# Kernel optimization log

Measured on AMD Instinct MI355X. Metric: run time of the kernel, lower is better.

## Reference

```python
import jax, jax.numpy as jnp
import numpy as np

VOCAB, EMBED, HIDDEN = 50257, 256, 512
BATCH, SEQ = 4, 2048


def posneg(x):
    # max(0,x) - |min(0,x)|  (mathematically the identity, computed as written)
    return jnp.maximum(jnp.zeros_like(x), x) - jnp.abs(jnp.minimum(jnp.zeros_like(x), x))


def setup_inputs() -> dict:
    key = jax.random.key(0)
    ks = jax.random.split(key, 10)
    s = 0.02
    return {
        "token_ids": jax.random.randint(ks[0], (BATCH, SEQ), 0, VOCAB),
        "emb_table": jax.random.normal(ks[1], (VOCAB, EMBED), jnp.float32) * s,
        "W1": jax.random.normal(ks[2], (EMBED, HIDDEN), jnp.float32) * s,
        "b1": jax.random.normal(ks[3], (HIDDEN,), jnp.float32) * s,
        "Wq": jax.random.normal(ks[4], (HIDDEN, HIDDEN), jnp.float32) * s,
        "bq": jax.random.normal(ks[5], (HIDDEN,), jnp.float32) * s,
        "Wk": jax.random.normal(ks[6], (HIDDEN, HIDDEN), jnp.float32) * s,
        "bk": jax.random.normal(ks[7], (HIDDEN,), jnp.float32) * s,
        "Wv": jax.random.normal(ks[8], (HIDDEN, HIDDEN), jnp.float32) * s,
        "bv": jax.random.normal(ks[9], (HIDDEN,), jnp.float32) * s,
    }


def reference(token_ids, emb_table, W1, b1, Wq, bq, Wk, bk, Wv, bv):
    emb = emb_table[token_ids]                      # [B,S,E]
    emb = posneg(emb)
    hidden = posneg(emb) @ W1 + b1                  # [B,S,H]
    hidden = posneg(hidden)
    act = jax.nn.gelu(hidden, approximate=False)
    act = posneg(act)
    q = posneg(act) @ Wq + bq
    k = posneg(act) @ Wk + bk
    v = posneg(act) @ Wv + bv
    q, k, v = posneg(q), posneg(k), posneg(v)
    # scaled_dot_product_attention (single head, hand-rolled)
    q, k = posneg(q), posneg(k)
    scores = jnp.einsum("bsh,bth->bst", q, k)       # [B,S,S]
    scores = posneg(scores) / jnp.sqrt(jnp.float32(q.shape[-1]))
    attn = jax.nn.softmax(scores, axis=-1)
    attn = posneg(attn)
    v = posneg(v)
    out = jnp.einsum("bst,bth->bsh", attn, v)       # [B,S,H]
    return posneg(out)
```

## Files before the change

kernel.cpp:

```cpp
#include <hip/hip_runtime.h>
#include <math.h>


typedef unsigned short u16;
typedef u16   u16x8 __attribute__((ext_vector_type(8)));
typedef short s16x8 __attribute__((ext_vector_type(8)));
typedef float f32x4 __attribute__((ext_vector_type(4)));
typedef float f32x8 __attribute__((ext_vector_type(8)));

static __device__ __forceinline__ u16 f2bf(float f) {
    unsigned u = __builtin_bit_cast(unsigned, f);
    u = (u + 0x7fffu + ((u >> 16) & 1u)) >> 16;
    return (u16)u;
}
static __device__ __forceinline__ float bf2f(u16 h) {
    unsigned u = ((unsigned)h) << 16;
    return __builtin_bit_cast(float, u);
}

static __device__ __forceinline__ void gload_lds16(const u16* g, u16* l) {
    __builtin_amdgcn_global_load_lds(
        (const __attribute__((address_space(1))) void*)g,
        (__attribute__((address_space(3))) void*)l, 16, 0, 0);
}

__launch_bounds__(256)
__global__ void cvt_gather_k(const float* __restrict__ emb, const int* __restrict__ tok,
                             u16* __restrict__ dst)
{
    const int b = blockIdx.x;
    const int g = (b & 7) * 128 + (b >> 3);
    const int t = g * 2048 + threadIdx.x * 8;
    const int row = t >> 8;
    const int c8  = t & 255;
    f32x8 v = *(const f32x8*)(emb + (long)tok[row] * 256 + c8);
    u16x8 o;
#pragma unroll
    for (int j = 0; j < 8; ++j) o[j] = f2bf(v[j]);
    *(u16x8*)(dst + (long)row * 256 + c8) = o;
}

struct WArgs {
    const float* src[4];
    u16*         dst[4];
    int          K[4];
};

__launch_bounds__(256)
__global__ void transpose_w_k(WArgs wa)
{
    const int w = blockIdx.z;
    const float* W = wa.src[w];
    u16* WT = wa.dst[w];
    const int K = wa.K[w];
    const int c0 = blockIdx.x * 64;
    const int r0 = blockIdx.y * 64;
    if (r0 >= K) return;

    __shared__ float T[64][65];
    const int t = threadIdx.x;
    const int col = t & 63;
    const int rb  = t >> 6;

#pragma unroll
    for (int i = 0; i < 16; ++i)
        T[i * 4 + rb][col] = W[(long)(r0 + i * 4 + rb) * 512 + c0 + col];
    __syncthreads();
#pragma unroll
    for (int i = 0; i < 16; ++i) {
        const int orow = i * 4 + rb;
        WT[(long)(c0 + orow) * K + r0 + col] = f2bf(T[col][orow]);
    }
}

__launch_bounds__(256)
__global__ void transpose_v_k(const u16* __restrict__ v, u16* __restrict__ vT)
{
    const int b  = blockIdx.z;
    const int h0 = blockIdx.x * 64;
    const int t0 = blockIdx.y * 64;

    __shared__ u16 T[64][65];
    const int t = threadIdx.x;
    const int col = t & 63;
    const int rb  = t >> 6;

#pragma unroll
    for (int i = 0; i < 16; ++i) {
        const int row = i * 4 + rb;
        T[row][col] = v[(long)(b * 2048 + t0 + row) * 512 + h0 + col];
    }
    __syncthreads();
#pragma unroll
    for (int i = 0; i < 16; ++i) {
        const int orow = i * 4 + rb;
        vT[(long)b * (512 * 2048) + (long)(h0 + orow) * 2048 + t0 + col] = T[col][orow];
    }
}

struct GArgs {
    const u16* A; const u16* B; const float* bias; void* C;
    float* Cpart;
    u16 *qd, *kd, *vd;
    const float *bq, *bk, *bv;
    int K, lda, ldb, ldc;
    long strA, strB, strC;
    float scale;
};

template <int TM, int EPI, int CMODE, bool MX, bool SPLITK, bool XSW>
__launch_bounds__(256)
__global__ void gemm128(GArgs g)
{
    constexpr int BM  = TM * 32;
    constexpr int ASZ = BM * 32;
    constexpr int BSZ = 128 * 32;
    __shared__ u16 As[2 * ASZ];
    __shared__ u16 Bs[2 * BSZ];

    const int bz    = blockIdx.z;
    const int batch = SPLITK ? (bz >> 1) : bz;
    const int kh    = SPLITK ? (bz & 1) : 0;
    const u16* A = g.A + g.strA * batch + (SPLITK ? kh * 1024 : 0);
    const u16* B = g.B + g.strB * batch + (SPLITK ? kh * 1024 : 0);

    int m0, n0;
    if (XSW) {
        const int lid = blockIdx.y * gridDim.x + blockIdx.x;
        const int xcd = lid & 7;
        const int j   = lid >> 3;
        const int mper = gridDim.y >> 3;
        m0 = (xcd * mper + (j % mper)) * BM;
        n0 = (j / mper) * 128;
    } else {
        m0 = (MX ? blockIdx.x : blockIdx.y) * BM;
        n0 = (MX ? blockIdx.y : blockIdx.x) * 128;
    }

    const int t = threadIdx.x;
    const int w = t >> 6;
    const int lane = t & 63;
    const int quad = lane >> 4;
    const int l16  = lane & 15;
    const int wm = w >> 1, wn = w & 1;

    const int srow = w * 16 + (lane >> 2);
    const int skc  = (lane & 3) * 8;
    const u16* ga = A + (long)(m0 + srow) * g.lda + skc;
    const u16* gb = B + (long)(n0 + srow) * g.ldb + skc;
    const long a64 = (long)64 * g.lda;
    const long b64 = (long)64 * g.ldb;
    u16* lA = As + w * 512;
    u16* lB = Bs + w * 512;

    auto stage = [&](int buf, int k0) {
        u16* la = lA + buf * ASZ;
        u16* lb = lB + buf * BSZ;
        gload_lds16(ga + k0, la);
        if (TM == 4) gload_lds16(ga + a64 + k0, la + 2048);
        gload_lds16(gb + k0, lb);
        gload_lds16(gb + b64 + k0, lb + 2048);
    };

    f32x4 acc[TM][4] = {};
    const int K = SPLITK ? 1024 : g.K;

    stage(0, 0);
    int cur = 0;
    for (int k0 = 0; k0 < K; k0 += 32) {
        __syncthreads();
        if (k0 + 32 < K) stage(cur ^ 1, k0 + 32);

        const u16* as = As + cur * ASZ;
        const u16* bs = Bs + cur * BSZ;
        s16x8 af[TM], bf[4];
#pragma unroll
        for (int x = 0; x < TM; ++x)
            af[x] = *(const s16x8*)&as[(wm * (TM * 16) + x * 16 + l16) * 32 + quad * 8];
#pragma unroll
        for (int y = 0; y < 4; ++y)
            bf[y] = *(const s16x8*)&bs[(wn * 64 + y * 16 + l16) * 32 + quad * 8];
#pragma unroll
        for (int x = 0; x < TM; ++x)
#pragma unroll
            for (int y = 0; y < 4; ++y)
                acc[x][y] = __builtin_amdgcn_mfma_f32_16x16x32_bf16(af[x], bf[y], acc[x][y], 0, 0, 0);
        cur ^= 1;
    }

#pragma unroll
    for (int y = 0; y < 4; ++y) {
        const int col = n0 + wn * 64 + y * 16 + l16;
        float bval = 0.0f;
        if (CMODE == 2)
            bval = col < 512 ? g.bq[col] : (col < 1024 ? g.bk[col - 512] : g.bv[col - 1024]);
        else if (EPI >= 1)
            bval = g.bias[col];
#pragma unroll
        for (int x = 0; x < TM; ++x) {
#pragma unroll
            for (int r = 0; r < 4; ++r) {
                const int row = m0 + wm * (TM * 16) + x * 16 + quad * 4 + r;
                float v = acc[x][y][r] * g.scale + bval;
                if (EPI == 2) v = 0.5f * v * (1.0f + erff(v * 0.70710678118654752f));
                if (CMODE == 2) {
                    u16* dst = col < 512 ? g.qd : (col < 1024 ? g.kd : g.vd);
                    const int c = col & 511;
                    dst[(long)row * 512 + c] = f2bf(v);
                } else if (SPLITK) {
                    float* dst = kh ? g.Cpart : (float*)g.C;
                    dst[g.strC * batch + (long)row * g.ldc + col] = v;
                } else if (CMODE == 1) {
                    ((float*)g.C + g.strC * batch)[(long)row * g.ldc + col] = v;
                } else {
                    ((u16*)g.C + g.strC * batch)[(long)row * g.ldc + col] = f2bf(v);
                }
            }
        }
    }
}

__launch_bounds__(256)
__global__ void softmax_k(u16* __restrict__ sc)
{
    const long base = (long)blockIdx.x * 2048;
    const int t = threadIdx.x;
    const int wid = t >> 6, lane = t & 63;
    __shared__ float redm[4];
    __shared__ float reds[4];

    float v[8];
    float mx = -1e30f;
#pragma unroll
    for (int i = 0; i < 8; ++i) {
        v[i] = bf2f(sc[base + i * 256 + t]);
        mx = fmaxf(mx, v[i]);
    }
#pragma unroll
    for (int off = 32; off; off >>= 1) mx = fmaxf(mx, __shfl_xor(mx, off, 64));
    if (lane == 0) redm[wid] = mx;
    __syncthreads();
    const float bm = fmaxf(fmaxf(redm[0], redm[1]), fmaxf(redm[2], redm[3]));

    float s = 0.0f;
#pragma unroll
    for (int i = 0; i < 8; ++i) { v[i] = expf(v[i] - bm); s += v[i]; }
#pragma unroll
    for (int off = 32; off; off >>= 1) s += __shfl_xor(s, off, 64);
    if (lane == 0) reds[wid] = s;
    __syncthreads();
    const float inv = 1.0f / (reds[0] + reds[1] + reds[2] + reds[3]);

#pragma unroll
    for (int i = 0; i < 8; ++i) sc[base + i * 256 + t] = f2bf(v[i] * inv);
}

__launch_bounds__(256)
__global__ void add_k(float* __restrict__ out, const float* __restrict__ part)
{
    const long i = ((long)blockIdx.x * 256 + threadIdx.x) * 4;
    f32x4 a = *(const f32x4*)(out + i);
    f32x4 b = *(const f32x4*)(part + i);
    a += b;
    *(f32x4*)(out + i) = a;
}

extern "C" void kernel_launch(void* const* d_in, const int* in_sizes, int n_in,
                              void* d_out, int out_size, void* d_ws, size_t ws_size,
                              hipStream_t stream)
{
    const int*   tok = (const int*)d_in[0];
    const float* emb = (const float*)d_in[1];
    const float* W1  = (const float*)d_in[2];
    const float* b1  = (const float*)d_in[3];
    const float* Wq  = (const float*)d_in[4];
    const float* bq  = (const float*)d_in[5];
    const float* Wk  = (const float*)d_in[6];
    const float* bk  = (const float*)d_in[7];
    const float* Wv  = (const float*)d_in[8];
    const float* bv  = (const float*)d_in[9];
    float* out = (float*)d_out;

    u16* act   = (u16*)d_out;
    u16* wbase = act + 8192l * 512;
    u16* W1T = wbase;
    u16* WqT = wbase + 131072;
    u16* WkT = WqT + 262144;
    u16* WvT = WkT + 262144;

    char* ws = (char*)d_ws;
    u16* q    = (u16*)(ws);
    u16* k    = (u16*)(ws + (8l  << 20));
    u16* vT   = (u16*)(ws + (16l << 20));
    u16* sc   = (u16*)(ws + (24l << 20));
    u16* embB = sc;
    u16* vrow = sc;
    float* wsP = (float*)ws;

    const dim3 blk(256);
    const float iscl = 0.044194173824159216f;
    const long  TB = 2048l * 512;
    const long  SS = 2048l * 2048;

    cvt_gather_k<<<dim3(1024), blk, 0, stream>>>(emb, tok, embB);
    WArgs wa;
    wa.src[0] = W1; wa.src[1] = Wq; wa.src[2] = Wk; wa.src[3] = Wv;
    wa.dst[0] = W1T; wa.dst[1] = WqT; wa.dst[2] = WkT; wa.dst[3] = WvT;
    wa.K[0] = 256; wa.K[1] = 512; wa.K[2] = 512; wa.K[3] = 512;
    transpose_w_k<<<dim3(8, 8, 4), blk, 0, stream>>>(wa);

    {
        GArgs a = {};
        a.A = embB; a.B = W1T; a.bias = b1; a.C = act;
        a.K = 256; a.lda = 256; a.ldb = 256; a.ldc = 512; a.scale = 1.0f;
        gemm128<2, 2, 0, false, false, true><<<dim3(4, 128, 1), blk, 0, stream>>>(a);
    }
    {
        GArgs a = {};
        a.A = act; a.B = WqT; a.K = 512; a.lda = 512; a.ldb = 512; a.scale = 1.0f;
        a.qd = q; a.kd = k; a.vd = vrow; a.bq = bq; a.bk = bk; a.bv = bv;
        gemm128<2, 0, 2, false, false, true><<<dim3(12, 128, 1), blk, 0, stream>>>(a);
    }
    transpose_v_k<<<dim3(8, 32, 4), blk, 0, stream>>>(vrow, vT);
    {
        GArgs a = {};
        a.A = q; a.B = k; a.C = sc;
        a.K = 512; a.lda = 512; a.ldb = 512; a.ldc = 2048;
        a.strA = TB; a.strB = TB; a.strC = SS; a.scale = iscl;
        gemm128<4, 0, 0, false, false, false><<<dim3(16, 16, 4), blk, 0, stream>>>(a);
    }
    softmax_k<<<dim3(8192), blk, 0, stream>>>(sc);
    {
        GArgs a = {};
        a.A = sc; a.B = vT; a.C = out; a.Cpart = wsP;
        a.K = 2048; a.lda = 2048; a.ldb = 2048; a.ldc = 512;
        a.strA = SS; a.strB = TB; a.strC = TB; a.scale = 1.0f;
        gemm128<2, 0, 1, true, true, false><<<dim3(32, 4, 8), blk, 0, stream>>>(a);
    }
    add_k<<<dim3(4096), blk, 0, stream>>>(out, wsP);
}
```

Before: 231.4 us.

## Widen GEMM N-tiles, merge prep kernels, use fast exp in softmax

The GEMM template gains an NT parameter, so the QKV, QK^T and PV GEMMs now use 256-wide N tiles with more accumulators per wave and half as many blocks. This raises B-tile reuse and cuts A-tile reloads. The embedding gather and weight transposes are merged into one prep launch, saving a launch. Softmax switches to __expf. The trade-off is higher register pressure: the launch-bounds hint of 2 blocks per SM may cause spills, and fewer blocks may underfill the CUs.

```diff
diff --git a/kernel.cpp b/kernel.cpp
--- a/kernel.cpp
+++ b/kernel.cpp
@@ -24,52 +24,50 @@
         (__attribute__((address_space(3))) void*)l, 16, 0, 0);
 }
 
+struct PArgs {
+    const float* wsrc[4];
+    u16*         wdst[4];
+    int          wK[4];
+    const float* emb;
+    const int*   tok;
+    u16*         embB;
+};
+
 __launch_bounds__(256)
-__global__ void cvt_gather_k(const float* __restrict__ emb, const int* __restrict__ tok,
-                             u16* __restrict__ dst)
-{
-    const int b = blockIdx.x;
-    const int g = (b & 7) * 128 + (b >> 3);
-    const int t = g * 2048 + threadIdx.x * 8;
-    const int row = t >> 8;
-    const int c8  = t & 255;
-    f32x8 v = *(const f32x8*)(emb + (long)tok[row] * 256 + c8);
-    u16x8 o;
-#pragma unroll
-    for (int j = 0; j < 8; ++j) o[j] = f2bf(v[j]);
-    *(u16x8*)(dst + (long)row * 256 + c8) = o;
-}
-
-struct WArgs {
-    const float* src[4];
-    u16*         dst[4];
-    int          K[4];
-};
-
-__launch_bounds__(256)
-__global__ void transpose_w_k(WArgs wa)
-{
-    const int w = blockIdx.z;
-    const float* W = wa.src[w];
-    u16* WT = wa.dst[w];
-    const int K = wa.K[w];
-    const int c0 = blockIdx.x * 64;
-    const int r0 = blockIdx.y * 64;
-    if (r0 >= K) return;
-
-    __shared__ float T[64][65];
-    const int t = threadIdx.x;
-    const int col = t & 63;
-    const int rb  = t >> 6;
-
-#pragma unroll
-    for (int i = 0; i < 16; ++i)
-        T[i * 4 + rb][col] = W[(long)(r0 + i * 4 + rb) * 512 + c0 + col];
-    __syncthreads();
-#pragma unroll
-    for (int i = 0; i < 16; ++i) {
-        const int orow = i * 4 + rb;
-        WT[(long)(c0 + orow) * K + r0 + col] = f2bf(T[col][orow]);
+__global__ void prep_k(PArgs p)
+{
+    const int z = blockIdx.z;
+    if (z < 4) {
+        const float* W = p.wsrc[z];
+        u16* WT = p.wdst[z];
+        const int K = p.wK[z];
+        const int c0 = blockIdx.x * 64;
+        const int r0 = blockIdx.y * 64;
+        if (r0 >= K) return;
+        __shared__ float T[64][65];
+        const int t = threadIdx.x;
+        const int col = t & 63;
+        const int rb  = t >> 6;
+#pragma unroll
+        for (int i = 0; i < 16; ++i)
+            T[i * 4 + rb][col] = W[(long)(r0 + i * 4 + rb) * 512 + c0 + col];
+        __syncthreads();
+#pragma unroll
+        for (int i = 0; i < 16; ++i) {
+            const int orow = i * 4 + rb;
+            WT[(long)(c0 + orow) * K + r0 + col] = f2bf(T[col][orow]);
+        }
+    } else {
+        const int b = (z - 4) * 64 + blockIdx.y * 8 + blockIdx.x;
+        const int g = (b & 7) * 128 + (b >> 3);
+        const int t = g * 2048 + threadIdx.x * 8;
+        const int row = t >> 8;
+        const int c8  = t & 255;
+        f32x8 v = *(const f32x8*)(p.emb + (long)p.tok[row] * 256 + c8);
+        u16x8 o;
+#pragma unroll
+        for (int j = 0; j < 8; ++j) o[j] = f2bf(v[j]);
+        *(u16x8*)(p.embB + (long)row * 256 + c8) = o;
     }
 }
 
@@ -79,17 +77,13 @@
     const int b  = blockIdx.z;
     const int h0 = blockIdx.x * 64;
     const int t0 = blockIdx.y * 64;
-
     __shared__ u16 T[64][65];
     const int t = threadIdx.x;
     const int col = t & 63;
     const int rb  = t >> 6;
-
-#pragma unroll
-    for (int i = 0; i < 16; ++i) {
-        const int row = i * 4 + rb;
-        T[row][col] = v[(long)(b * 2048 + t0 + row) * 512 + h0 + col];
-    }
+#pragma unroll
+    for (int i = 0; i < 16; ++i)
+        T[i * 4 + rb][col] = v[(long)(b * 2048 + t0 + i * 4 + rb) * 512 + h0 + col];
     __syncthreads();
 #pragma unroll
     for (int i = 0; i < 16; ++i) {
@@ -108,13 +102,14 @@
     float scale;
 };
 
-template <int TM, int EPI, int CMODE, bool MX, bool SPLITK, bool XSW>
-__launch_bounds__(256)
+template <int TM, int NT, int EPI, int CMODE, bool MX, bool SPLITK, bool XSW>
+__launch_bounds__(256, 2)
 __global__ void gemm128(GArgs g)
 {
     constexpr int BM  = TM * 32;
+    constexpr int BN  = NT * 32;
     constexpr int ASZ = BM * 32;
-    constexpr int BSZ = 128 * 32;
+    constexpr int BSZ = BN * 32;
     __shared__ u16 As[2 * ASZ];
     __shared__ u16 Bs[2 * BSZ];
 
@@ -131,10 +126,10 @@
         const int j   = lid >> 3;
         const int mper = gridDim.y >> 3;
         m0 = (xcd * mper + (j % mper)) * BM;
-        n0 = (j / mper) * 128;
+        n0 = (j / mper) * BN;
     } else {
         m0 = (MX ? blockIdx.x : blockIdx.y) * BM;
-        n0 = (MX ? blockIdx.y : blockIdx.x) * 128;
+        n0 = (MX ? blockIdx.y : blockIdx.x) * BN;
     }
 
     const int t = threadIdx.x;
@@ -156,13 +151,13 @@
     auto stage = [&](int buf, int k0) {
         u16* la = lA + buf * ASZ;
         u16* lb = lB + buf * BSZ;
-        gload_lds16(ga + k0, la);
-        if (TM == 4) gload_lds16(ga + a64 + k0, la + 2048);
-        gload_lds16(gb + k0, lb);
-        gload_lds16(gb + b64 + k0, lb + 2048);
+#pragma unroll
+        for (int i = 0; i < TM / 2; ++i) gload_lds16(ga + i * a64 + k0, la + i * 2048);
+#pragma unroll
+        for (int i = 0; i < NT / 2; ++i) gload_lds16(gb + i * b64 + k0, lb + i * 2048);
     };
 
-    f32x4 acc[TM][4] = {};
+    f32x4 acc[TM][NT] = {};
     const int K = SPLITK ? 1024 : g.K;
 
     stage(0, 0);
@@ -173,24 +168,24 @@
 
         const u16* as = As + cur * ASZ;
         const u16* bs = Bs + cur * BSZ;
-        s16x8 af[TM], bf[4];
+        s16x8 af[TM], bf[NT];
 #pragma unroll
         for (int x = 0; x < TM; ++x)
             af[x] = *(const s16x8*)&as[(wm * (TM * 16) + x * 16 + l16) * 32 + quad * 8];
 #pragma unroll
-        for (int y = 0; y < 4; ++y)
-            bf[y] = *(const s16x8*)&bs[(wn * 64 + y * 16 + l16) * 32 + quad * 8];
+        for (int y = 0; y < NT; ++y)
+            bf[y] = *(const s16x8*)&bs[(wn * (NT * 16) + y * 16 + l16) * 32 + quad * 8];
 #pragma unroll
         for (int x = 0; x < TM; ++x)
 #pragma unroll
-            for (int y = 0; y < 4; ++y)
+            for (int y = 0; y < NT; ++y)
                 acc[x][y] = __builtin_amdgcn_mfma_f32_16x16x32_bf16(af[x], bf[y], acc[x][y], 0, 0, 0);
         cur ^= 1;
     }
 
 #pragma unroll
-    for (int y = 0; y < 4; ++y) {
-        const int col = n0 + wn * 64 + y * 16 + l16;
+    for (int y = 0; y < NT; ++y) {
+        const int col = n0 + wn * (NT * 16) + y * 16 + l16;
         float bval = 0.0f;
         if (CMODE == 2)
             bval = col < 512 ? g.bq[col] : (col < 1024 ? g.bk[col - 512] : g.bv[col - 1024]);
@@ -205,8 +200,7 @@
                 if (EPI == 2) v = 0.5f * v * (1.0f + erff(v * 0.70710678118654752f));
                 if (CMODE == 2) {
                     u16* dst = col < 512 ? g.qd : (col < 1024 ? g.kd : g.vd);
-                    const int c = col & 511;
-                    dst[(long)row * 512 + c] = f2bf(v);
+                    dst[(long)row * 512 + (col & 511)] = f2bf(v);
                 } else if (SPLITK) {
                     float* dst = kh ? g.Cpart : (float*)g.C;
                     dst[g.strC * batch + (long)row * g.ldc + col] = v;
@@ -244,7 +238,7 @@
 
     float s = 0.0f;
 #pragma unroll
-    for (int i = 0; i < 8; ++i) { v[i] = expf(v[i] - bm); s += v[i]; }
+    for (int i = 0; i < 8; ++i) { v[i] = __expf(v[i] - bm); s += v[i]; }
 #pragma unroll
     for (int off = 32; off; off >>= 1) s += __shfl_xor(s, off, 64);
     if (lane == 0) reds[wid] = s;
@@ -302,24 +296,24 @@
     const long  TB = 2048l * 512;
     const long  SS = 2048l * 2048;
 
-    cvt_gather_k<<<dim3(1024), blk, 0, stream>>>(emb, tok, embB);
-    WArgs wa;
-    wa.src[0] = W1; wa.src[1] = Wq; wa.src[2] = Wk; wa.src[3] = Wv;
-    wa.dst[0] = W1T; wa.dst[1] = WqT; wa.dst[2] = WkT; wa.dst[3] = WvT;
-    wa.K[0] = 256; wa.K[1] = 512; wa.K[2] = 512; wa.K[3] = 512;
-    transpose_w_k<<<dim3(8, 8, 4), blk, 0, stream>>>(wa);
+    PArgs p;
+    p.wsrc[0] = W1; p.wsrc[1] = Wq; p.wsrc[2] = Wk; p.wsrc[3] = Wv;
+    p.wdst[0] = W1T; p.wdst[1] = WqT; p.wdst[2] = WkT; p.wdst[3] = WvT;
+    p.wK[0] = 256; p.wK[1] = 512; p.wK[2] = 512; p.wK[3] = 512;
+    p.emb = emb; p.tok = tok; p.embB = embB;
+    prep_k<<<dim3(8, 8, 20), blk, 0, stream>>>(p);
 
     {
         GArgs a = {};
         a.A = embB; a.B = W1T; a.bias = b1; a.C = act;
         a.K = 256; a.lda = 256; a.ldb = 256; a.ldc = 512; a.scale = 1.0f;
-        gemm128<2, 2, 0, false, false, true><<<dim3(4, 128, 1), blk, 0, stream>>>(a);
+        gemm128<2, 4, 2, 0, false, false, true><<<dim3(4, 128, 1), blk, 0, stream>>>(a);
     }
     {
         GArgs a = {};
         a.A = act; a.B = WqT; a.K = 512; a.lda = 512; a.ldb = 512; a.scale = 1.0f;
         a.qd = q; a.kd = k; a.vd = vrow; a.bq = bq; a.bk = bk; a.bv = bv;
-        gemm128<2, 0, 2, false, false, true><<<dim3(12, 128, 1), blk, 0, stream>>>(a);
+        gemm128<2, 8, 0, 2, false, false, true><<<dim3(6, 128, 1), blk, 0, stream>>>(a);
     }
     transpose_v_k<<<dim3(8, 32, 4), blk, 0, stream>>>(vrow, vT);
     {
@@ -327,7 +321,7 @@
         a.A = q; a.B = k; a.C = sc;
         a.K = 512; a.lda = 512; a.ldb = 512; a.ldc = 2048;
         a.strA = TB; a.strB = TB; a.strC = SS; a.scale = iscl;
-        gemm128<4, 0, 0, false, false, false><<<dim3(16, 16, 4), blk, 0, stream>>>(a);
+        gemm128<4, 8, 0, 0, false, false, false><<<dim3(8, 16, 4), blk, 0, stream>>>(a);
     }
     softmax_k<<<dim3(8192), blk, 0, stream>>>(sc);
     {
@@ -335,7 +329,7 @@
         a.A = sc; a.B = vT; a.C = out; a.Cpart = wsP;
         a.K = 2048; a.lda = 2048; a.ldb = 2048; a.ldc = 512;
         a.strA = SS; a.strB = TB; a.strC = TB; a.scale = 1.0f;
-        gemm128<2, 0, 1, true, true, false><<<dim3(32, 4, 8), blk, 0, stream>>>(a);
+        gemm128<2, 8, 0, 1, true, true, false><<<dim3(32, 2, 8), blk, 0, stream>>>(a);
     }
     add_k<<<dim3(4096), blk, 0, stream>>>(out, wsP);
 }
```

Result: faster. 219.0 us (-5.3%).
